# Performance work log

Hardware: AMD Instinct MI355X
Metric: run time of the kernel (lower is better)

Reference implementation:

```python
import jax, jax.numpy as jnp
import numpy as np
import math

B, S, D = 2, 2048, 1024
H, KV, HD = 16, 4, 64
N_REP = H // KV
ROPE_THETA = 1.0e6


def _rope_tables(seq_len, head_dim, theta):
    inv_freq = 1.0 / (theta ** (np.arange(0, head_dim, 2, dtype=np.float32) / head_dim))
    t = np.arange(seq_len, dtype=np.float32)
    freqs = np.outer(t, inv_freq)                      # [S, HD/2]
    emb = np.concatenate([freqs, freqs], axis=-1)      # [S, HD]
    return jnp.asarray(np.cos(emb)), jnp.asarray(np.sin(emb))


def setup_inputs() -> dict:
    key = jax.random.key(0)
    ks = jax.random.split(key, 6)
    cos, sin = _rope_tables(S, HD, ROPE_THETA)
    scale = 0.02
    return {
        "x": jax.random.normal(ks[0], (B, S, D), dtype=jnp.float32),
        "cos": cos,
        "sin": sin,
        "Wq": jax.random.normal(ks[1], (D, H * HD), dtype=jnp.float32) * scale,
        "Wk": jax.random.normal(ks[2], (D, KV * HD), dtype=jnp.float32) * scale,
        "Wv": jax.random.normal(ks[3], (D, KV * HD), dtype=jnp.float32) * scale,
        "Wo": jax.random.normal(ks[4], (H * HD, D), dtype=jnp.float32) * scale,
    }


def _rotate_half(u):
    u1, u2 = u[..., : HD // 2], u[..., HD // 2 :]
    return jnp.concatenate([-u2, u1], axis=-1)


def reference(x, cos, sin, Wq, Wk, Wv, Wo):
    bsz, seq_len, _ = x.shape
    q = (x @ Wq).reshape(bsz, seq_len, H, HD)   # [B,S,H,HD]
    k = (x @ Wk).reshape(bsz, seq_len, KV, HD)  # [B,S,KV,HD]
    v = (x @ Wv).reshape(bsz, seq_len, KV, HD)

    # RoPE: cos/sin [S,HD] broadcast over batch and heads (unsqueeze_dim=1)
    c = cos[:seq_len][None, :, None, :]
    s = sin[:seq_len][None, :, None, :]
    q = q * c + _rotate_half(q) * s
    k = k * c + _rotate_half(k) * s

    # repeat_kv: expand KV heads groupwise to H heads
    k = jnp.repeat(k, N_REP, axis=2)  # [B,S,H,HD]
    v = jnp.repeat(v, N_REP, axis=2)

    q = q.transpose(0, 2, 1, 3)  # [B,H,S,HD]
    k = k.transpose(0, 2, 1, 3)
    v = v.transpose(0, 2, 1, 3)

    scores = jnp.einsum("bhqd,bhkd->bhqk", q, k) / math.sqrt(HD)
    causal = jnp.tril(jnp.ones((seq_len, seq_len), dtype=bool))
    scores = jnp.where(causal[None, None], scores, jnp.finfo(jnp.float32).min)
    probs = jax.nn.softmax(scores.astype(jnp.float32), axis=-1).astype(x.dtype)

    out = jnp.einsum("bhqk,bhkd->bhqd", probs, v)        # [B,H,S,HD]
    out = out.transpose(0, 2, 1, 3).reshape(bsz, seq_len, H * HD)
    return out @ Wo
```

## Files before the change

### kernel.cpp

```cpp
#include <hip/hip_runtime.h>

#define SS 2048
#define NH 16
#define NKV 4
#define HD 64

typedef __bf16 bf16;
typedef __bf16 bf16x4 __attribute__((ext_vector_type(4)));
typedef __bf16 bf16x8 __attribute__((ext_vector_type(8)));
typedef float f32x4 __attribute__((ext_vector_type(4)));

#define SM_SCALE 0.18033688011f

__device__ __forceinline__ void gl_lds16(const bf16* g, bf16* l) {
    __builtin_amdgcn_global_load_lds((const __attribute__((address_space(1))) void*)g,
                                     (__attribute__((address_space(3))) void*)l, 16, 0, 0);
}

__global__ __launch_bounds__(256) void prep_kernel(
    const float* __restrict__ x,
    const float* __restrict__ Wq, const float* __restrict__ Wk,
    const float* __restrict__ Wv, const float* __restrict__ Wo,
    bf16* __restrict__ wqkv_t, bf16* __restrict__ wo_t, bf16* __restrict__ xb)
{
    const int blk = blockIdx.x;
    const int tid = threadIdx.x;
    if (blk >= 640) {
        const size_t i0 = (size_t)(blk - 640) * 16384;
        #pragma unroll
        for (int i = 0; i < 16; ++i) {
            const size_t idx = i0 + i * 1024 + tid * 4;
            const float4 v = *(const float4*)&x[idx];
            bf16x4 o4;
            o4[0] = (bf16)v.x; o4[1] = (bf16)v.y; o4[2] = (bf16)v.z; o4[3] = (bf16)v.w;
            *(bf16x4*)&xb[idx] = o4;
        }
        return;
    }
    const float* W; bf16* Wt; int N, n0, k0;
    if (blk < 256)      { W = Wq; Wt = wqkv_t;                       N = 1024; n0 = (blk & 15) * 64;         k0 = (blk >> 4) * 64; }
    else if (blk < 320) { W = Wk; Wt = wqkv_t + (size_t)1024 * 1024; N = 256;  n0 = ((blk - 256) & 3) * 64;  k0 = ((blk - 256) >> 2) * 64; }
    else if (blk < 384) { W = Wv; Wt = wqkv_t + (size_t)1280 * 1024; N = 256;  n0 = ((blk - 320) & 3) * 64;  k0 = ((blk - 320) >> 2) * 64; }
    else                { W = Wo; Wt = wo_t;                         N = 1024; n0 = ((blk - 384) & 15) * 64; k0 = ((blk - 384) >> 4) * 64; }

    __shared__ float Ts[64][65];
    const int c = tid & 63, rr = tid >> 6;
    #pragma unroll
    for (int i = 0; i < 16; ++i) {
        const int kk = i * 4 + rr;
        Ts[kk][c] = W[(size_t)(k0 + kk) * N + n0 + c];
    }
    __syncthreads();
    #pragma unroll
    for (int i = 0; i < 16; ++i) {
        const int nn = i * 4 + rr;
        Wt[(size_t)(n0 + nn) * 1024 + k0 + c] = (bf16)Ts[c][nn];
    }
}

template<int EPI>
__global__ __launch_bounds__(512) void gemm_bt_kernel(
    const bf16* __restrict__ A, const bf16* __restrict__ Bt, float* __restrict__ C,
    const float* __restrict__ cosp, const float* __restrict__ sinp,
    bf16* __restrict__ qo, bf16* __restrict__ ko, bf16* __restrict__ vto,
    int N, int K, int CB)
{
    __shared__ bf16 As[2][128 * 64];
    __shared__ bf16 Bs[2][128 * 64];
    const int bid = blockIdx.x;
    const int j = bid >> 3;
    const int rb = (bid & 7) + 8 * (j / CB);
    const int cb = j % CB;
    const int m0 = rb * 128, n0 = cb * 128;
    const int tid = threadIdx.x;
    const int w = tid >> 6, lane = tid & 63, g = lane >> 4, li = lane & 15;
    const int wm = w >> 1, wn = w & 1;

    f32x4 acc[2][4];
    const f32x4 z = {0.f, 0.f, 0.f, 0.f};
    #pragma unroll
    for (int i = 0; i < 2; ++i)
        #pragma unroll
        for (int jj = 0; jj < 4; ++jj) acc[i][jj] = z;

    const int srow = tid >> 3;
    const int schunk = ((tid & 7) ^ (srow & 7)) * 8;
    const bf16* pA[2];
    const bf16* pB[2];
    #pragma unroll
    for (int s = 0; s < 2; ++s) {
        pA[s] = A  + (size_t)(m0 + s * 64 + srow) * K + schunk;
        pB[s] = Bt + (size_t)(n0 + s * 64 + srow) * K + schunk;
    }
    const int lw = w * 512;

    const int NT = K >> 6;

    #pragma unroll
    for (int s = 0; s < 2; ++s) gl_lds16(pA[s], &As[0][s * 4096 + lw]);
    #pragma unroll
    for (int s = 0; s < 2; ++s) gl_lds16(pB[s], &Bs[0][s * 4096 + lw]);
    #pragma unroll
    for (int s = 0; s < 2; ++s) gl_lds16(pA[s] + 64, &As[1][s * 4096 + lw]);
    #pragma unroll
    for (int s = 0; s < 2; ++s) gl_lds16(pB[s] + 64, &Bs[1][s * 4096 + lw]);

    for (int t = 0; t < NT; ++t) {
        const int cur = t & 1;
        if (t + 1 < NT) { asm volatile("s_waitcnt vmcnt(4)" ::: "memory"); }
        else            { asm volatile("s_waitcnt vmcnt(0)" ::: "memory"); }
        __builtin_amdgcn_s_barrier();
        #pragma unroll
        for (int tt = 0; tt < 2; ++tt) {
            const int phys = ((tt * 4 + g) ^ (li & 7)) * 8;
            bf16x8 af[2], bfr[4];
            #pragma unroll
            for (int mi = 0; mi < 2; ++mi) af[mi] = *(const bf16x8*)&As[cur][(wm * 32 + mi * 16 + li) * 64 + phys];
            #pragma unroll
            for (int ni = 0; ni < 4; ++ni) bfr[ni] = *(const bf16x8*)&Bs[cur][(wn * 64 + ni * 16 + li) * 64 + phys];
            __builtin_amdgcn_s_setprio(1);
            #pragma unroll
            for (int mi = 0; mi < 2; ++mi)
                #pragma unroll
                for (int ni = 0; ni < 4; ++ni)
                    acc[mi][ni] = __builtin_amdgcn_mfma_f32_16x16x32_bf16(af[mi], bfr[ni], acc[mi][ni], 0, 0, 0);
            __builtin_amdgcn_s_setprio(0);
        }
        __builtin_amdgcn_s_barrier();
        if (t + 2 < NT) {
            const int kk = (t + 2) << 6;
            #pragma unroll
            for (int s = 0; s < 2; ++s) gl_lds16(pA[s] + kk, &As[cur][s * 4096 + lw]);
            #pragma unroll
            for (int s = 0; s < 2; ++s) gl_lds16(pB[s] + kk, &Bs[cur][s * 4096 + lw]);
        }
    }

    const int row0 = m0 + wm * 32, col0 = n0 + wn * 64;
    if (EPI == 0) {
        #pragma unroll
        for (int mi = 0; mi < 2; ++mi)
            #pragma unroll
            for (int ni = 0; ni < 4; ++ni)
                #pragma unroll
                for (int r = 0; r < 4; ++r)
                    C[(size_t)(row0 + mi * 16 + g * 4 + r) * N + col0 + ni * 16 + li] = acc[mi][ni][r];
    } else {
        #pragma unroll
        for (int ni = 0; ni < 4; ++ni) {
            const int col = col0 + ni * 16 + li;
            const int d = col & 63;
            #pragma unroll
            for (int mi = 0; mi < 2; ++mi) {
                #pragma unroll
                for (int r = 0; r < 4; ++r) {
                    const int row = row0 + mi * 16 + g * 4 + r;
                    const int bb = row >> 11, s = row & 2047;
                    float val = acc[mi][ni][r];
                    if (col < 1280) {
                        const float pairv = acc[mi][ni ^ 2][r];
                        const float rot = (d < 32) ? -pairv : pairv;
                        val = val * cosp[s * 64 + d] + rot * sinp[s * 64 + d];
                    }
                    if (col < 1024) {
                        const int hh = col >> 6;
                        qo[(((size_t)bb * NH + hh) * SS + s) * HD + d] = (bf16)(val * SM_SCALE);
                    } else if (col < 1280) {
                        const int kh = (col - 1024) >> 6;
                        ko[(((size_t)bb * NKV + kh) * SS + s) * HD + d] = (bf16)val;
                    } else {
                        const int kh = (col - 1280) >> 6;
                        vto[(((size_t)bb * NKV + kh) * HD + d) * SS + s] = (bf16)val;
                    }
                }
            }
        }
    }
}

__global__ __launch_bounds__(256) void flash_kernel(const bf16* __restrict__ q, const bf16* __restrict__ k,
                                                    const bf16* __restrict__ vt, bf16* __restrict__ o)
{
    __shared__ bf16 Ks[2][64 * 64];
    __shared__ bf16 Vt[2][64 * 64];
    __shared__ bf16 Ps[4][16 * 64];

    const int blk = blockIdx.x;
    const int qt = 31 - (blk >> 5);
    const int h = blk & 15;
    const int b = (blk >> 4) & 1;
    const int kvh = h >> 2;
    const int tid = threadIdx.x;
    const int w = tid >> 6, lane = tid & 63, g = lane >> 4, li = lane & 15;

    const bf16* qh = q + ((size_t)b * NH + h) * SS * HD;
    const bf16* kh = k + ((size_t)b * NKV + kvh) * SS * HD;
    const bf16* vh = vt + ((size_t)b * NKV + kvh) * (size_t)HD * SS;

    bf16x8 ones;
    #pragma unroll
    for (int jj = 0; jj < 8; ++jj) ones[jj] = (bf16)1.0f;
    const f32x4 z = {0.f, 0.f, 0.f, 0.f};

    const bf16* qrow = qh + (size_t)(qt * 64 + w * 16 + li) * HD;
    bf16x8 qf[2];
    qf[0] = *(const bf16x8*)(qrow + g * 8);
    qf[1] = *(const bf16x8*)(qrow + 32 + g * 8);

    const int srow = tid >> 3;
    const int schunk = ((tid & 7) ^ (srow & 7)) * 8;
    const int lw = w * 512;

    const int xm = (li & 7) << 1;

    f32x4 o_acc[4], l_acc;
    #pragma unroll
    for (int nt = 0; nt < 4; ++nt) o_acc[nt] = z;
    l_acc = z;

    #pragma unroll
    for (int s = 0; s < 2; ++s)
        gl_lds16(kh + (size_t)(s * 32 + srow) * HD + schunk, &Ks[0][s * 2048 + lw]);
    #pragma unroll
    for (int s = 0; s < 2; ++s)
        gl_lds16(vh + (size_t)(s * 32 + srow) * SS + schunk, &Vt[0][s * 2048 + lw]);
    if (qt >= 1) {
        #pragma unroll
        for (int s = 0; s < 2; ++s)
            gl_lds16(kh + (size_t)(64 + s * 32 + srow) * HD + schunk, &Ks[1][s * 2048 + lw]);
        #pragma unroll
        for (int s = 0; s < 2; ++s)
            gl_lds16(vh + (size_t)(s * 32 + srow) * SS + 64 + schunk, &Vt[1][s * 2048 + lw]);
    }

    for (int kt = 0; kt <= qt; ++kt) {
        const int cur = kt & 1;
        if (kt < qt) { asm volatile("s_waitcnt vmcnt(4)" ::: "memory"); }
        else         { asm volatile("s_waitcnt vmcnt(0)" ::: "memory"); }
        __builtin_amdgcn_s_barrier();

        f32x4 s_acc[4];
        #pragma unroll
        for (int nt = 0; nt < 4; ++nt) s_acc[nt] = z;
        __builtin_amdgcn_s_setprio(1);
        #pragma unroll
        for (int t = 0; t < 2; ++t)
            #pragma unroll
            for (int nt = 0; nt < 4; ++nt) {
                const bf16x8 kf = *(const bf16x8*)&Ks[cur][(nt * 16 + li) * 64 + (((t * 4 + g) ^ (li & 7)) * 8)];
                s_acc[nt] = __builtin_amdgcn_mfma_f32_16x16x32_bf16(kf, qf[t], s_acc[nt], 0, 0, 0);
            }
        __builtin_amdgcn_s_setprio(0);

        if (kt == qt) {
            const int qrow_in = w * 16 + li;
            #pragma unroll
            for (int nt = 0; nt < 4; ++nt) {
                bf16x4 p4;
                #pragma unroll
                for (int r = 0; r < 4; ++r) {
                    float sv = s_acc[nt][r];
                    if (nt * 16 + g * 4 + r > qrow_in) sv = -1e30f;
                    p4[r] = (bf16)exp2f(sv);
                }
                *(bf16x4*)&Ps[w][li * 64 + (((nt * 4 + g) ^ xm) * 4)] = p4;
            }
        } else {
            #pragma unroll
            for (int nt = 0; nt < 4; ++nt) {
                bf16x4 p4;
                #pragma unroll
                for (int r = 0; r < 4; ++r) p4[r] = (bf16)exp2f(s_acc[nt][r]);
                *(bf16x4*)&Ps[w][li * 64 + (((nt * 4 + g) ^ xm) * 4)] = p4;
            }
        }

        __builtin_amdgcn_s_setprio(1);
        #pragma unroll
        for (int t = 0; t < 2; ++t) {
            const bf16x8 pf = *(const bf16x8*)&Ps[w][li * 64 + (((t * 8 + g * 2) ^ xm) * 4)];
            l_acc = __builtin_amdgcn_mfma_f32_16x16x32_bf16(pf, ones, l_acc, 0, 0, 0);
            #pragma unroll
            for (int nt = 0; nt < 4; ++nt) {
                const bf16x8 vf = *(const bf16x8*)&Vt[cur][(nt * 16 + li) * 64 + (((t * 4 + g) ^ (li & 7)) * 8)];
                o_acc[nt] = __builtin_amdgcn_mfma_f32_16x16x32_bf16(pf, vf, o_acc[nt], 0, 0, 0);
            }
        }
        __builtin_amdgcn_s_setprio(0);

        __builtin_amdgcn_s_barrier();
        if (kt + 2 <= qt) {
            const size_t kq = (size_t)(kt + 2) * 64;
            #pragma unroll
            for (int s = 0; s < 2; ++s)
                gl_lds16(kh + (kq + s * 32 + srow) * HD + schunk, &Ks[cur][s * 2048 + lw]);
            #pragma unroll
            for (int s = 0; s < 2; ++s)
                gl_lds16(vh + (size_t)(s * 32 + srow) * SS + kq + schunk, &Vt[cur][s * 2048 + lw]);
        }
    }

    #pragma unroll
    for (int r = 0; r < 4; ++r) {
        const float inv = 1.f / l_acc[r];
        const int s = qt * 64 + w * 16 + g * 4 + r;
        bf16* orow = o + (((size_t)b * SS + s) * NH + h) * HD;
        #pragma unroll
        for (int nt = 0; nt < 4; ++nt) orow[nt * 16 + li] = (bf16)(o_acc[nt][r] * inv);
    }
}

extern "C" void kernel_launch(void* const* d_in, const int* in_sizes, int n_in,
                              void* d_out, int out_size, void* d_ws, size_t ws_size,
                              hipStream_t stream) {
    const float* x     = (const float*)d_in[0];
    const float* cos_t = (const float*)d_in[1];
    const float* sin_t = (const float*)d_in[2];
    const float* Wq    = (const float*)d_in[3];
    const float* Wk    = (const float*)d_in[4];
    const float* Wv    = (const float*)d_in[5];
    const float* Wo    = (const float*)d_in[6];
    float* out = (float*)d_out;

    char* wsb = (char*)d_ws;
    bf16* o_b    = (bf16*)(wsb);
    bf16* wqkv_t = (bf16*)(wsb + 8388608);
    bf16* wo_t   = (bf16*)(wsb + 11534336);
    bf16* q_b    = (bf16*)(wsb + 13631488);
    bf16* k_b    = (bf16*)(wsb + 22020096);
    bf16* vt_b   = (bf16*)(wsb + 24117248);
    bf16* x_b    = (bf16*)(wsb + 26214400);

    prep_kernel<<<896, 256, 0, stream>>>(x, Wq, Wk, Wv, Wo, wqkv_t, wo_t, x_b);

    gemm_bt_kernel<2><<<384, 512, 0, stream>>>(x_b, wqkv_t, nullptr, cos_t, sin_t,
                                               q_b, k_b, vt_b, 1536, 1024, 12);
    flash_kernel<<<1024, 256, 0, stream>>>(q_b, k_b, vt_b, o_b);
    gemm_bt_kernel<0><<<256, 512, 0, stream>>>(o_b, wo_t, out, nullptr, nullptr,
                                               nullptr, nullptr, nullptr, 1024, 1024, 8);
}
```

Baseline: 168.7 us.

## Double query tile per block in flash kernel to reuse K/V tiles

Each flash-attention block now handles 128 query rows instead of 64: each wave computes two 16-row sub-tiles that share the K and V fragments loaded from LDS, and the grid is halved to 512 blocks. This halves the global K/V traffic per query row and the number of LDS fragment loads per MFMA. The cost is more registers per wave for accumulators, fewer blocks to fill the GPU, and some waves sitting idle on the diagonal tiles where their rows are fully masked.

```diff
diff --git a/kernel.cpp b/kernel.cpp
--- a/kernel.cpp
+++ b/kernel.cpp
@@ -183,10 +183,10 @@
 {
     __shared__ bf16 Ks[2][64 * 64];
     __shared__ bf16 Vt[2][64 * 64];
-    __shared__ bf16 Ps[4][16 * 64];
+    __shared__ bf16 Ps[4][2][16 * 64];
 
     const int blk = blockIdx.x;
-    const int qt = 31 - (blk >> 5);
+    const int qt = 15 - (blk >> 5);
     const int h = blk & 15;
     const int b = (blk >> 4) & 1;
     const int kvh = h >> 2;
@@ -202,10 +202,14 @@
     for (int jj = 0; jj < 8; ++jj) ones[jj] = (bf16)1.0f;
     const f32x4 z = {0.f, 0.f, 0.f, 0.f};
 
-    const bf16* qrow = qh + (size_t)(qt * 64 + w * 16 + li) * HD;
-    bf16x8 qf[2];
-    qf[0] = *(const bf16x8*)(qrow + g * 8);
-    qf[1] = *(const bf16x8*)(qrow + 32 + g * 8);
+    const int wrow0 = qt * 128 + w * 32;
+    bf16x8 qf[2][2];
+    #pragma unroll
+    for (int mi = 0; mi < 2; ++mi) {
+        const bf16* qrow = qh + (size_t)(wrow0 + mi * 16 + li) * HD;
+        qf[mi][0] = *(const bf16x8*)(qrow + g * 8);
+        qf[mi][1] = *(const bf16x8*)(qrow + 32 + g * 8);
+    }
 
     const int srow = tid >> 3;
     const int schunk = ((tid & 7) ^ (srow & 7)) * 8;
@@ -213,10 +217,15 @@
 
     const int xm = (li & 7) << 1;
 
-    f32x4 o_acc[4], l_acc;
-    #pragma unroll
-    for (int nt = 0; nt < 4; ++nt) o_acc[nt] = z;
-    l_acc = z;
+    const int nkt = 2 * qt + 2;
+
+    f32x4 o_acc[2][4], l_acc[2];
+    #pragma unroll
+    for (int mi = 0; mi < 2; ++mi) {
+        #pragma unroll
+        for (int nt = 0; nt < 4; ++nt) o_acc[mi][nt] = z;
+        l_acc[mi] = z;
+    }
 
     #pragma unroll
     for (int s = 0; s < 2; ++s)
@@ -224,72 +233,87 @@
     #pragma unroll
     for (int s = 0; s < 2; ++s)
         gl_lds16(vh + (size_t)(s * 32 + srow) * SS + schunk, &Vt[0][s * 2048 + lw]);
-    if (qt >= 1) {
-        #pragma unroll
-        for (int s = 0; s < 2; ++s)
-            gl_lds16(kh + (size_t)(64 + s * 32 + srow) * HD + schunk, &Ks[1][s * 2048 + lw]);
-        #pragma unroll
-        for (int s = 0; s < 2; ++s)
-            gl_lds16(vh + (size_t)(s * 32 + srow) * SS + 64 + schunk, &Vt[1][s * 2048 + lw]);
-    }
-
-    for (int kt = 0; kt <= qt; ++kt) {
+    #pragma unroll
+    for (int s = 0; s < 2; ++s)
+        gl_lds16(kh + (size_t)(64 + s * 32 + srow) * HD + schunk, &Ks[1][s * 2048 + lw]);
+    #pragma unroll
+    for (int s = 0; s < 2; ++s)
+        gl_lds16(vh + (size_t)(s * 32 + srow) * SS + 64 + schunk, &Vt[1][s * 2048 + lw]);
+
+    for (int kt = 0; kt < nkt; ++kt) {
         const int cur = kt & 1;
-        if (kt < qt) { asm volatile("s_waitcnt vmcnt(4)" ::: "memory"); }
-        else         { asm volatile("s_waitcnt vmcnt(0)" ::: "memory"); }
+        if (kt + 1 < nkt) { asm volatile("s_waitcnt vmcnt(4)" ::: "memory"); }
+        else              { asm volatile("s_waitcnt vmcnt(0)" ::: "memory"); }
         __builtin_amdgcn_s_barrier();
 
-        f32x4 s_acc[4];
-        #pragma unroll
-        for (int nt = 0; nt < 4; ++nt) s_acc[nt] = z;
-        __builtin_amdgcn_s_setprio(1);
-        #pragma unroll
-        for (int t = 0; t < 2; ++t)
-            #pragma unroll
-            for (int nt = 0; nt < 4; ++nt) {
-                const bf16x8 kf = *(const bf16x8*)&Ks[cur][(nt * 16 + li) * 64 + (((t * 4 + g) ^ (li & 7)) * 8)];
-                s_acc[nt] = __builtin_amdgcn_mfma_f32_16x16x32_bf16(kf, qf[t], s_acc[nt], 0, 0, 0);
+        if (kt * 64 <= wrow0 + 31) {
+            f32x4 s_acc[2][4];
+            #pragma unroll
+            for (int mi = 0; mi < 2; ++mi)
+                #pragma unroll
+                for (int nt = 0; nt < 4; ++nt) s_acc[mi][nt] = z;
+            __builtin_amdgcn_s_setprio(1);
+            #pragma unroll
+            for (int t = 0; t < 2; ++t)
+                #pragma unroll
+                for (int nt = 0; nt < 4; ++nt) {
+                    const bf16x8 kf = *(const bf16x8*)&Ks[cur][(nt * 16 + li) * 64 + (((t * 4 + g) ^ (li & 7)) * 8)];
+                    #pragma unroll
+                    for (int mi = 0; mi < 2; ++mi)
+                        s_acc[mi][nt] = __builtin_amdgcn_mfma_f32_16x16x32_bf16(kf, qf[mi][t], s_acc[mi][nt], 0, 0, 0);
+                }
+            __builtin_amdgcn_s_setprio(0);
+
+            if (kt >= 2 * qt) {
+                #pragma unroll
+                for (int mi = 0; mi < 2; ++mi) {
+                    const int qrow = wrow0 + mi * 16 + li;
+                    #pragma unroll
+                    for (int nt = 0; nt < 4; ++nt) {
+                        bf16x4 p4;
+                        #pragma unroll
+                        for (int r = 0; r < 4; ++r) {
+                            float sv = s_acc[mi][nt][r];
+                            if (kt * 64 + nt * 16 + g * 4 + r > qrow) sv = -1e30f;
+                            p4[r] = (bf16)exp2f(sv);
+                        }
+                        *(bf16x4*)&Ps[w][mi][li * 64 + (((nt * 4 + g) ^ xm) * 4)] = p4;
+                    }
+                }
+            } else {
+                #pragma unroll
+                for (int mi = 0; mi < 2; ++mi)
+                    #pragma unroll
+                    for (int nt = 0; nt < 4; ++nt) {
+                        bf16x4 p4;
+                        #pragma unroll
+                        for (int r = 0; r < 4; ++r) p4[r] = (bf16)exp2f(s_acc[mi][nt][r]);
+                        *(bf16x4*)&Ps[w][mi][li * 64 + (((nt * 4 + g) ^ xm) * 4)] = p4;
+                    }
             }
-        __builtin_amdgcn_s_setprio(0);
-
-        if (kt == qt) {
-            const int qrow_in = w * 16 + li;
-            #pragma unroll
-            for (int nt = 0; nt < 4; ++nt) {
-                bf16x4 p4;
-                #pragma unroll
-                for (int r = 0; r < 4; ++r) {
-                    float sv = s_acc[nt][r];
-                    if (nt * 16 + g * 4 + r > qrow_in) sv = -1e30f;
-                    p4[r] = (bf16)exp2f(sv);
-                }
-                *(bf16x4*)&Ps[w][li * 64 + (((nt * 4 + g) ^ xm) * 4)] = p4;
+
+            __builtin_amdgcn_s_setprio(1);
+            #pragma unroll
+            for (int t = 0; t < 2; ++t) {
+                bf16x8 pf[2];
+                #pragma unroll
+                for (int mi = 0; mi < 2; ++mi) {
+                    pf[mi] = *(const bf16x8*)&Ps[w][mi][li * 64 + (((t * 8 + g * 2) ^ xm) * 4)];
+                    l_acc[mi] = __builtin_amdgcn_mfma_f32_16x16x32_bf16(pf[mi], ones, l_acc[mi], 0, 0, 0);
+                }
+                #pragma unroll
+                for (int nt = 0; nt < 4; ++nt) {
+                    const bf16x8 vf = *(const bf16x8*)&Vt[cur][(nt * 16 + li) * 64 + (((t * 4 + g) ^ (li & 7)) * 8)];
+                    #pragma unroll
+                    for (int mi = 0; mi < 2; ++mi)
+                        o_acc[mi][nt] = __builtin_amdgcn_mfma_f32_16x16x32_bf16(pf[mi], vf, o_acc[mi][nt], 0, 0, 0);
+                }
             }
-        } else {
-            #pragma unroll
-            for (int nt = 0; nt < 4; ++nt) {
-                bf16x4 p4;
-                #pragma unroll
-                for (int r = 0; r < 4; ++r) p4[r] = (bf16)exp2f(s_acc[nt][r]);
-                *(bf16x4*)&Ps[w][li * 64 + (((nt * 4 + g) ^ xm) * 4)] = p4;
-            }
-        }
-
-        __builtin_amdgcn_s_setprio(1);
-        #pragma unroll
-        for (int t = 0; t < 2; ++t) {
-            const bf16x8 pf = *(const bf16x8*)&Ps[w][li * 64 + (((t * 8 + g * 2) ^ xm) * 4)];
-            l_acc = __builtin_amdgcn_mfma_f32_16x16x32_bf16(pf, ones, l_acc, 0, 0, 0);
-            #pragma unroll
-            for (int nt = 0; nt < 4; ++nt) {
-                const bf16x8 vf = *(const bf16x8*)&Vt[cur][(nt * 16 + li) * 64 + (((t * 4 + g) ^ (li & 7)) * 8)];
-                o_acc[nt] = __builtin_amdgcn_mfma_f32_16x16x32_bf16(pf, vf, o_acc[nt], 0, 0, 0);
-            }
-        }
-        __builtin_amdgcn_s_setprio(0);
+            __builtin_amdgcn_s_setprio(0);
+        }
 
         __builtin_amdgcn_s_barrier();
-        if (kt + 2 <= qt) {
+        if (kt + 2 < nkt) {
             const size_t kq = (size_t)(kt + 2) * 64;
             #pragma unroll
             for (int s = 0; s < 2; ++s)
@@ -301,13 +325,15 @@
     }
 
     #pragma unroll
-    for (int r = 0; r < 4; ++r) {
-        const float inv = 1.f / l_acc[r];
-        const int s = qt * 64 + w * 16 + g * 4 + r;
-        bf16* orow = o + (((size_t)b * SS + s) * NH + h) * HD;
-        #pragma unroll
-        for (int nt = 0; nt < 4; ++nt) orow[nt * 16 + li] = (bf16)(o_acc[nt][r] * inv);
-    }
+    for (int mi = 0; mi < 2; ++mi)
+        #pragma unroll
+        for (int r = 0; r < 4; ++r) {
+            const float inv = 1.f / l_acc[mi][r];
+            const int s = wrow0 + mi * 16 + g * 4 + r;
+            bf16* orow = o + (((size_t)b * SS + s) * NH + h) * HD;
+            #pragma unroll
+            for (int nt = 0; nt < 4; ++nt) orow[nt * 16 + li] = (bf16)(o_acc[mi][nt][r] * inv);
+        }
 }
 
 extern "C" void kernel_launch(void* const* d_in, const int* in_sizes, int n_in,
@@ -335,7 +361,7 @@
 
     gemm_bt_kernel<2><<<384, 512, 0, stream>>>(x_b, wqkv_t, nullptr, cos_t, sin_t,
                                                q_b, k_b, vt_b, 1536, 1024, 12);
-    flash_kernel<<<1024, 256, 0, stream>>>(q_b, k_b, vt_b, o_b);
+    flash_kernel<<<512, 256, 0, stream>>>(q_b, k_b, vt_b, o_b);
     gemm_bt_kernel<0><<<256, 512, 0, stream>>>(o_b, wo_t, out, nullptr, nullptr,
                                                nullptr, nullptr, nullptr, 1024, 1024, 8);
 }
```

After: 183.0 us. +8.5%, slower.
